# Kernel tuning notes

Hardware: AMD Instinct MI355X
Metric: run time of the kernel (lower is better)

## Reference

```python
import jax, jax.numpy as jnp
import numpy as np

D_IN, D_SAE, T, L, K = 2304, 2048, 4, 6, 128
B = 32


def setup_inputs() -> dict:
    key = jax.random.key(0)
    kx, ke, kd = jax.random.split(key, 3)
    x = jax.random.normal(kx, (B, T, L, D_IN), dtype=jnp.float32)
    W_enc = jax.random.normal(ke, (T, L, D_IN, D_SAE), dtype=jnp.float32) / np.sqrt(D_IN).astype(np.float32)
    W_dec = jax.random.normal(kd, (T, L, D_SAE, D_IN), dtype=jnp.float32) / np.sqrt(D_SAE).astype(np.float32)
    b_enc = jnp.zeros((D_SAE,), dtype=jnp.float32)
    b_dec = jnp.zeros((T, L, D_IN), dtype=jnp.float32)
    return {"x": x, "W_enc": W_enc, "W_dec": W_dec, "b_enc": b_enc, "b_dec": b_dec}


def reference(x, W_enc, W_dec, b_enc, b_dec):
    # encode: per-(t,l) matmul, pre: (B, T, L, d_sae)
    pre = jnp.einsum('btld,tlds->btls', x, W_enc) + b_enc
    Bn = pre.shape[0]
    pre_flat = pre.reshape(Bn, T * L * D_SAE)
    # global TopK over the whole (T, L, d_sae) latent grid
    v, idx = jax.lax.top_k(pre_flat, K)
    z_flat = jnp.zeros_like(pre_flat).at[jnp.arange(Bn)[:, None], idx].set(jax.nn.relu(v))
    z = z_flat.reshape(Bn, T, L, D_SAE)
    # decode: per-(t,l) matmul
    x_hat = jnp.einsum('btls,tlsd->btld', z, W_dec) + b_dec
    loss = jnp.mean(jnp.sum(jnp.square(x_hat - x), axis=-1))
    return (loss, x_hat, z)
```

## Files before the change

kernel.cpp:

```cpp
#include <hip/hip_runtime.h>

#define D_IN   2304
#define D_SAE  2048
#define TL     24
#define BATCH  32
#define K_TOP  128
#define NLAT   (TL * D_SAE)
#define NBIN   8192
#define CAP    2048
#define KSPLIT 2
#define KS     (D_IN / KSPLIT)
#define BK     32
#define NCH    (KS / BK)

typedef __attribute__((ext_vector_type(8))) short short8;
typedef __attribute__((ext_vector_type(4))) float f32x4;

__device__ __forceinline__ void async_cp16(const float* g, float* l) {
    __builtin_amdgcn_global_load_lds(
        (const __attribute__((address_space(1))) unsigned int*)g,
        (__attribute__((address_space(3))) unsigned int*)l, 16, 0, 0);
}

__device__ __forceinline__ void cvt8(const float* f, short8& hi, short8& lo) {
#pragma unroll
    for (int j = 0; j < 8; ++j) {
        unsigned u = __float_as_uint(f[j]);
        hi[j] = (short)(u >> 16);
        float l = f[j] - __uint_as_float(u & 0xFFFF0000u);
        lo[j] = (short)(__float_as_uint(l) >> 16);
    }
}

__global__ __launch_bounds__(256, 3) void enc_kernel(const float* __restrict__ x,
                                                     const float* __restrict__ W,
                                                     float* __restrict__ part) {
    __shared__ float w_s[2][BK][128];
    __shared__ float x_s[2][32][36];

    const int tid  = threadIdx.x;
    const int lane = tid & 63;
    const int wv   = tid >> 6;
    const int m0   = lane & 15;
    const int kb   = lane >> 4;
    const int tl   = blockIdx.y;
    const int ks   = blockIdx.z;
    const int n0b  = blockIdx.x * 128;
    const int kb0  = ks * KS;

    const float* Wbase = W + ((size_t)(tl * D_IN + kb0)) * D_SAE + n0b;
    const int xb = tid >> 3, xq = (tid & 7) * 4;
    const float* xsrc = x + ((size_t)(xb * TL + tl)) * D_IN + kb0 + xq;

#define STAGE_W(buf, ch)                                                        \
    do {                                                                        \
        const float* Wc = Wbase + (size_t)((ch) * BK) * D_SAE;                  \
        _Pragma("unroll")                                                       \
        for (int j = 0; j < 4; ++j) {                                           \
            int r = wv * 8 + j * 2;                                             \
            async_cp16(Wc + (size_t)(r + (lane >> 5)) * D_SAE + (lane & 31) * 4,\
                       &w_s[buf][r][0]);                                        \
        }                                                                       \
    } while (0)

    f32x4 acc[2][2];
#pragma unroll
    for (int mt = 0; mt < 2; ++mt)
#pragma unroll
        for (int nt = 0; nt < 2; ++nt) acc[mt][nt] = (f32x4)(0.f);

    {
        float4 xr = *(const float4*)xsrc;
        STAGE_W(0, 0);
        asm volatile("s_waitcnt vmcnt(0)" ::: "memory");
        *(float4*)&x_s[0][xb][xq] = xr;
        __syncthreads();
    }

    int cur = 0;
    for (int ch = 0; ch < NCH; ++ch) {
        float4 xr;
        if (ch + 1 < NCH) {
            xr = *(const float4*)(xsrc + (ch + 1) * BK);
            STAGE_W(cur ^ 1, ch + 1);
        }

        const float(*ws)[128] = w_s[cur];
        const float(*xs)[36]  = x_s[cur];
        short8 ahi[2], alo[2];
#pragma unroll
        for (int mt = 0; mt < 2; ++mt) {
            float xa[8];
            *(float4*)&xa[0] = *(const float4*)&xs[mt * 16 + m0][kb * 8];
            *(float4*)&xa[4] = *(const float4*)&xs[mt * 16 + m0][kb * 8 + 4];
            cvt8(xa, ahi[mt], alo[mt]);
        }
#pragma unroll
        for (int nt = 0; nt < 2; ++nt) {
            float wf[8];
#pragma unroll
            for (int j = 0; j < 8; ++j)
                wf[j] = ws[kb * 8 + j][wv * 32 + nt * 16 + m0];
            short8 bhi, blo;
            cvt8(wf, bhi, blo);
#pragma unroll
            for (int mt = 0; mt < 2; ++mt) {
                acc[mt][nt] = __builtin_amdgcn_mfma_f32_16x16x32_bf16(ahi[mt], bhi, acc[mt][nt], 0, 0, 0);
                acc[mt][nt] = __builtin_amdgcn_mfma_f32_16x16x32_bf16(ahi[mt], blo, acc[mt][nt], 0, 0, 0);
                acc[mt][nt] = __builtin_amdgcn_mfma_f32_16x16x32_bf16(alo[mt], bhi, acc[mt][nt], 0, 0, 0);
            }
        }

        if (ch + 1 < NCH) {
            asm volatile("s_waitcnt vmcnt(0)" ::: "memory");
            *(float4*)&x_s[cur ^ 1][xb][xq] = xr;
        }
        __syncthreads();
        cur ^= 1;
    }
#undef STAGE_W

    float* pp = part + ((size_t)ks * BATCH) * NLAT + (size_t)tl * D_SAE + n0b;
#pragma unroll
    for (int mt = 0; mt < 2; ++mt)
#pragma unroll
        for (int nt = 0; nt < 2; ++nt)
#pragma unroll
            for (int r = 0; r < 4; ++r)
                pp[(size_t)(mt * 16 + kb * 4 + r) * NLAT + wv * 32 + nt * 16 + m0] =
                    acc[mt][nt][r];
}

__global__ void reduce_kernel(const float* __restrict__ part,
                              const float* __restrict__ b_enc,
                              float* __restrict__ pre) {
    int i = (blockIdx.x * blockDim.x + threadIdx.x) * 4;
    const size_t S = (size_t)BATCH * NLAT;
    float4 v = *(const float4*)&b_enc[i & (D_SAE - 1)];
#pragma unroll
    for (int s = 0; s < KSPLIT; s++) {
        float4 p = *(const float4*)&part[i + s * S];
        v.x += p.x; v.y += p.y; v.z += p.z; v.w += p.w;
    }
    *(float4*)&pre[i] = v;
}

__global__ __launch_bounds__(256) void topk_kernel(const float* __restrict__ pre,
                                                   int* __restrict__ sel_idx,
                                                   float* __restrict__ sel_val,
                                                   float* __restrict__ z,
                                                   float* __restrict__ loss) {
    const int b   = blockIdx.x;
    const int tid = threadIdx.x;
    __shared__ unsigned hist[NBIN];
    __shared__ unsigned cand_key[CAP];
    __shared__ int      cand_idx[CAP];
    __shared__ unsigned tsum[256];
    __shared__ unsigned suf[256];
    __shared__ int s_T, s_hi, s_ccnt, s_sel;

    const float* row  = pre + (size_t)b * NLAT;
    float*       zrow = z   + (size_t)b * NLAT;
    for (int i = tid; i < NBIN; i += 256) hist[i] = 0;
    if (tid == 0) { s_ccnt = 0; s_sel = 0; if (b == 0) *loss = 0.f; }
    __syncthreads();

    for (int i = 4 * tid; i < NLAT; i += 1024) {
        float4 v = *(const float4*)&row[i];
#pragma unroll
        for (int j = 0; j < 4; j++) {
            unsigned u   = __float_as_uint(((const float*)&v)[j]);
            unsigned key = u ^ ((u >> 31) ? 0xFFFFFFFFu : 0x80000000u);
            atomicAdd(&hist[key >> 19], 1u);
        }
    }
    __syncthreads();

    unsigned local = 0;
    const int base = tid * (NBIN / 256);
    for (int j = 0; j < NBIN / 256; j++) local += hist[base + j];
    tsum[tid] = local;
    __syncthreads();
    if (tid == 0) {
        unsigned run = 0;
        for (int t = 255; t >= 0; t--) { suf[t] = run; run += tsum[t]; }
    }
    __syncthreads();
    if (suf[tid] < K_TOP && suf[tid] + tsum[tid] >= K_TOP) {
        unsigned c = suf[tid];
        for (int j = NBIN / 256 - 1; j >= 0; j--) {
            int bin = base + j;
            if (c + hist[bin] >= K_TOP) { s_T = bin; s_hi = (int)c; break; }
            c += hist[bin];
        }
    }
    __syncthreads();

    const int T = s_T;
    for (int i = 4 * tid; i < NLAT; i += 1024) {
        float4 v = *(const float4*)&row[i];
#pragma unroll
        for (int j = 0; j < 4; j++) {
            float f      = ((const float*)&v)[j];
            unsigned u   = __float_as_uint(f);
            unsigned key = u ^ ((u >> 31) ? 0xFFFFFFFFu : 0x80000000u);
            int bin      = (int)(key >> 19);
            float rl     = fmaxf(f, 0.f);
            float zval   = 0.f;
            if (bin > T) {
                int p = atomicAdd(&s_sel, 1);
                sel_idx[b * K_TOP + p] = i + j;
                sel_val[b * K_TOP + p] = rl;
                zval = rl;
            } else if (bin == T) {
                int p = atomicAdd(&s_ccnt, 1);
                if (p < CAP) { cand_key[p] = key; cand_idx[p] = i + j; }
            }
            zrow[i + j] = zval;
        }
    }
    __syncthreads();

    const int need = K_TOP - s_hi;
    const int nc   = min(s_ccnt, CAP);
    for (int c = tid; c < nc; c += 256) {
        unsigned kc = cand_key[c]; int ic = cand_idx[c];
        int rank = 0;
        for (int j = 0; j < nc; j++) {
            unsigned kj = cand_key[j]; int ij = cand_idx[j];
            rank += (kj > kc) || (kj == kc && ij < ic);
        }
        if (rank < need) {
            int p = atomicAdd(&s_sel, 1);
            float rl = fmaxf(row[ic], 0.f);
            sel_idx[b * K_TOP + p] = ic;
            sel_val[b * K_TOP + p] = rl;
            zrow[ic] = rl;
        }
    }
}

__global__ __launch_bounds__(256) void dec_kernel(const float* __restrict__ Wd,
                                                  const float* __restrict__ b_dec,
                                                  const float* __restrict__ x,
                                                  const int* __restrict__ sel_idx,
                                                  const float* __restrict__ sel_val,
                                                  float* __restrict__ xhat,
                                                  float* __restrict__ loss) {
    const int tl = blockIdx.x, b = blockIdx.y, tid = threadIdx.x;
    float acc[9];
#pragma unroll
    for (int r = 0; r < 9; r++) acc[r] = b_dec[tl * D_IN + tid + r * 256];

    __shared__ int   s_idx[K_TOP];
    __shared__ float s_val[K_TOP];
    if (tid < K_TOP) { s_idx[tid] = sel_idx[b * K_TOP + tid];
                       s_val[tid] = sel_val[b * K_TOP + tid]; }
    __syncthreads();

    for (int j = 0; j < K_TOP; j++) {
        int f = s_idx[j];
        if ((f >> 11) == tl) {
            float v = s_val[j];
            const float* wrow = Wd + (size_t)f * D_IN;
#pragma unroll
            for (int r = 0; r < 9; r++)
                acc[r] = fmaf(v, wrow[tid + r * 256], acc[r]);
        }
    }

    const float* xr = x    + ((size_t)b * TL + tl) * D_IN;
    float*       xo = xhat + ((size_t)b * TL + tl) * D_IN;
    float lsum = 0.f;
#pragma unroll
    for (int r = 0; r < 9; r++) {
        float d = acc[r] - xr[tid + r * 256];
        xo[tid + r * 256] = acc[r];
        lsum += d * d;
    }
    __shared__ float red[256];
    red[tid] = lsum; __syncthreads();
    for (int s = 128; s > 0; s >>= 1) {
        if (tid < s) red[tid] += red[tid + s];
        __syncthreads();
    }
    if (tid == 0) atomicAdd(loss, red[0] * (1.0f / (BATCH * TL)));
}

extern "C" void kernel_launch(void* const* d_in, const int* in_sizes, int n_in,
                              void* d_out, int out_size, void* d_ws, size_t ws_size,
                              hipStream_t stream) {
    const float* x     = (const float*)d_in[0];
    const float* W_enc = (const float*)d_in[1];
    const float* W_dec = (const float*)d_in[2];
    const float* b_enc = (const float*)d_in[3];
    const float* b_dec = (const float*)d_in[4];

    float* out  = (float*)d_out;
    float* loss = out;
    float* xhat = out + 1;
    float* z    = out + 1 + (size_t)BATCH * TL * D_IN;

    const size_t S = (size_t)BATCH * NLAT;
    float* part    = (float*)d_ws;
    float* pre     = part + (size_t)KSPLIT * S;
    int*   sel_idx = (int*)(pre + S);
    float* sel_val = (float*)(sel_idx + BATCH * K_TOP);

    enc_kernel<<<dim3(16, TL, KSPLIT), 256, 0, stream>>>(x, W_enc, part);
    reduce_kernel<<<(int)(S / 1024), 256, 0, stream>>>(part, b_enc, pre);
    topk_kernel<<<BATCH, 256, 0, stream>>>(pre, sel_idx, sel_val, z, loss);
    dec_kernel<<<dim3(TL, BATCH), 256, 0, stream>>>(W_dec, b_dec, x, sel_idx, sel_val,
                                                    xhat, loss);
}
```

Before: 167.2 us.

## Triple-buffer encoder W loads, read x directly to registers, widen top-k blocks

The encoder GEMM moves from double to triple buffering of W tiles in LDS, with partial vmcnt waits and a single barrier per chunk so loads stay two chunks ahead. The x operand is no longer staged through LDS; each lane loads its own fragment straight into registers. The top-k kernel goes from 256 to 512 threads per block to parallelise the histogram and scan passes over each batch row. The trade-off is more LDS and registers in the encoder, which may hurt occupancy. The loop also assumes NCH is a multiple of 3, which holds since NCH is 36.

```diff
diff --git a/kernel.cpp b/kernel.cpp
--- a/kernel.cpp
+++ b/kernel.cpp
@@ -12,6 +12,7 @@
 #define KS     (D_IN / KSPLIT)
 #define BK     32
 #define NCH    (KS / BK)
+#define TOPK_T 512
 
 typedef __attribute__((ext_vector_type(8))) short short8;
 typedef __attribute__((ext_vector_type(4))) float f32x4;
@@ -31,12 +32,16 @@
         lo[j] = (short)(__float_as_uint(l) >> 16);
     }
 }
+__device__ __forceinline__ void cvt44(float4 a, float4 b, short8& hi, short8& lo) {
+    float f[8];
+    *(float4*)&f[0] = a; *(float4*)&f[4] = b;
+    cvt8(f, hi, lo);
+}
 
 __global__ __launch_bounds__(256, 3) void enc_kernel(const float* __restrict__ x,
                                                      const float* __restrict__ W,
                                                      float* __restrict__ part) {
-    __shared__ float w_s[2][BK][128];
-    __shared__ float x_s[2][32][36];
+    __shared__ float w_s[3][BK][128];
 
     const int tid  = threadIdx.x;
     const int lane = tid & 63;
@@ -45,82 +50,78 @@
     const int kb   = lane >> 4;
     const int tl   = blockIdx.y;
     const int ks   = blockIdx.z;
-    const int n0b  = blockIdx.x * 128;
-    const int kb0  = ks * KS;
-
-    const float* Wbase = W + ((size_t)(tl * D_IN + kb0)) * D_SAE + n0b;
-    const int xb = tid >> 3, xq = (tid & 7) * 4;
-    const float* xsrc = x + ((size_t)(xb * TL + tl)) * D_IN + kb0 + xq;
-
-#define STAGE_W(buf, ch)                                                        \
+    const int col0 = blockIdx.x * 128;
+
+    const float* Wbase = W + ((size_t)(tl * D_IN + ks * KS)) * D_SAE + col0;
+    const float* xsrc0 = x + ((size_t)(m0 * TL + tl)) * D_IN + ks * KS + kb * 8;
+    const float* xsrc1 = x + ((size_t)((16 + m0) * TL + tl)) * D_IN + ks * KS + kb * 8;
+
+    float4 xr0[4], xr1[4], xr2[4];
+
+#define STAGE(BUF, CH)                                                          \
     do {                                                                        \
-        const float* Wc = Wbase + (size_t)((ch) * BK) * D_SAE;                  \
+        const float* Wc = Wbase + (size_t)(CH) * BK * D_SAE;                    \
         _Pragma("unroll")                                                       \
-        for (int j = 0; j < 4; ++j) {                                           \
-            int r = wv * 8 + j * 2;                                             \
-            async_cp16(Wc + (size_t)(r + (lane >> 5)) * D_SAE + (lane & 31) * 4,\
-                       &w_s[buf][r][0]);                                        \
+        for (int i = 0; i < 4; ++i)                                             \
+            async_cp16(Wc + (size_t)(wv * 8 + 2 * i + (lane >> 5)) * D_SAE      \
+                          + (lane & 31) * 4,                                    \
+                       &w_s[BUF][wv * 8 + 2 * i][0]);                           \
+        xr##BUF[0] = *(const float4*)(xsrc0 + (CH) * BK);                       \
+        xr##BUF[1] = *(const float4*)(xsrc0 + (CH) * BK + 4);                   \
+        xr##BUF[2] = *(const float4*)(xsrc1 + (CH) * BK);                       \
+        xr##BUF[3] = *(const float4*)(xsrc1 + (CH) * BK + 4);                   \
+    } while (0)
+
+    f32x4 acc[2][2];
+#pragma unroll
+    for (int mt = 0; mt < 2; ++mt)
+#pragma unroll
+        for (int nt = 0; nt < 2; ++nt) acc[mt][nt] = (f32x4)(0.f);
+
+#define COMPUTE(BUF)                                                            \
+    do {                                                                        \
+        const float(*ws)[128] = w_s[BUF];                                       \
+        short8 a0h, a0l, a1h, a1l;                                              \
+        cvt44(xr##BUF[0], xr##BUF[1], a0h, a0l);                                \
+        cvt44(xr##BUF[2], xr##BUF[3], a1h, a1l);                                \
+        _Pragma("unroll")                                                       \
+        for (int nt = 0; nt < 2; ++nt) {                                        \
+            float wf[8];                                                        \
+            _Pragma("unroll")                                                   \
+            for (int j = 0; j < 8; ++j)                                         \
+                wf[j] = ws[kb * 8 + j][wv * 32 + nt * 16 + m0];                 \
+            short8 bhi, blo;                                                    \
+            cvt8(wf, bhi, blo);                                                 \
+            acc[0][nt] = __builtin_amdgcn_mfma_f32_16x16x32_bf16(a0h, bhi, acc[0][nt], 0, 0, 0); \
+            acc[0][nt] = __builtin_amdgcn_mfma_f32_16x16x32_bf16(a0h, blo, acc[0][nt], 0, 0, 0); \
+            acc[0][nt] = __builtin_amdgcn_mfma_f32_16x16x32_bf16(a0l, bhi, acc[0][nt], 0, 0, 0); \
+            acc[1][nt] = __builtin_amdgcn_mfma_f32_16x16x32_bf16(a1h, bhi, acc[1][nt], 0, 0, 0); \
+            acc[1][nt] = __builtin_amdgcn_mfma_f32_16x16x32_bf16(a1h, blo, acc[1][nt], 0, 0, 0); \
+            acc[1][nt] = __builtin_amdgcn_mfma_f32_16x16x32_bf16(a1l, bhi, acc[1][nt], 0, 0, 0); \
         }                                                                       \
     } while (0)
 
-    f32x4 acc[2][2];
-#pragma unroll
-    for (int mt = 0; mt < 2; ++mt)
-#pragma unroll
-        for (int nt = 0; nt < 2; ++nt) acc[mt][nt] = (f32x4)(0.f);
-
-    {
-        float4 xr = *(const float4*)xsrc;
-        STAGE_W(0, 0);
-        asm volatile("s_waitcnt vmcnt(0)" ::: "memory");
-        *(float4*)&x_s[0][xb][xq] = xr;
-        __syncthreads();
-    }
-
-    int cur = 0;
-    for (int ch = 0; ch < NCH; ++ch) {
-        float4 xr;
-        if (ch + 1 < NCH) {
-            xr = *(const float4*)(xsrc + (ch + 1) * BK);
-            STAGE_W(cur ^ 1, ch + 1);
-        }
-
-        const float(*ws)[128] = w_s[cur];
-        const float(*xs)[36]  = x_s[cur];
-        short8 ahi[2], alo[2];
-#pragma unroll
-        for (int mt = 0; mt < 2; ++mt) {
-            float xa[8];
-            *(float4*)&xa[0] = *(const float4*)&xs[mt * 16 + m0][kb * 8];
-            *(float4*)&xa[4] = *(const float4*)&xs[mt * 16 + m0][kb * 8 + 4];
-            cvt8(xa, ahi[mt], alo[mt]);
-        }
-#pragma unroll
-        for (int nt = 0; nt < 2; ++nt) {
-            float wf[8];
-#pragma unroll
-            for (int j = 0; j < 8; ++j)
-                wf[j] = ws[kb * 8 + j][wv * 32 + nt * 16 + m0];
-            short8 bhi, blo;
-            cvt8(wf, bhi, blo);
-#pragma unroll
-            for (int mt = 0; mt < 2; ++mt) {
-                acc[mt][nt] = __builtin_amdgcn_mfma_f32_16x16x32_bf16(ahi[mt], bhi, acc[mt][nt], 0, 0, 0);
-                acc[mt][nt] = __builtin_amdgcn_mfma_f32_16x16x32_bf16(ahi[mt], blo, acc[mt][nt], 0, 0, 0);
-                acc[mt][nt] = __builtin_amdgcn_mfma_f32_16x16x32_bf16(alo[mt], bhi, acc[mt][nt], 0, 0, 0);
-            }
-        }
-
-        if (ch + 1 < NCH) {
-            asm volatile("s_waitcnt vmcnt(0)" ::: "memory");
-            *(float4*)&x_s[cur ^ 1][xb][xq] = xr;
-        }
-        __syncthreads();
-        cur ^= 1;
-    }
-#undef STAGE_W
-
-    float* pp = part + ((size_t)ks * BATCH) * NLAT + (size_t)tl * D_SAE + n0b;
+#define ITER(BUF, NXT, C)                                                       \
+    do {                                                                        \
+        if ((C) + 1 < NCH) { asm volatile("s_waitcnt vmcnt(8)" ::: "memory"); } \
+        else               { asm volatile("s_waitcnt vmcnt(0)" ::: "memory"); } \
+        __builtin_amdgcn_s_barrier();                                           \
+        if ((C) + 2 < NCH) STAGE(NXT, (C) + 2);                                 \
+        COMPUTE(BUF);                                                           \
+    } while (0)
+
+    STAGE(0, 0);
+    STAGE(1, 1);
+    for (int c3 = 0; c3 < NCH; c3 += 3) {
+        ITER(0, 2, c3);
+        ITER(1, 0, c3 + 1);
+        ITER(2, 1, c3 + 2);
+    }
+#undef ITER
+#undef COMPUTE
+#undef STAGE
+
+    float* pp = part + ((size_t)ks * BATCH) * NLAT + (size_t)tl * D_SAE + col0;
 #pragma unroll
     for (int mt = 0; mt < 2; ++mt)
 #pragma unroll
@@ -145,27 +146,27 @@
     *(float4*)&pre[i] = v;
 }
 
-__global__ __launch_bounds__(256) void topk_kernel(const float* __restrict__ pre,
-                                                   int* __restrict__ sel_idx,
-                                                   float* __restrict__ sel_val,
-                                                   float* __restrict__ z,
-                                                   float* __restrict__ loss) {
+__global__ __launch_bounds__(TOPK_T) void topk_kernel(const float* __restrict__ pre,
+                                                      int* __restrict__ sel_idx,
+                                                      float* __restrict__ sel_val,
+                                                      float* __restrict__ z,
+                                                      float* __restrict__ loss) {
     const int b   = blockIdx.x;
     const int tid = threadIdx.x;
     __shared__ unsigned hist[NBIN];
     __shared__ unsigned cand_key[CAP];
     __shared__ int      cand_idx[CAP];
-    __shared__ unsigned tsum[256];
-    __shared__ unsigned suf[256];
+    __shared__ unsigned tsum[TOPK_T];
+    __shared__ unsigned suf[TOPK_T];
     __shared__ int s_T, s_hi, s_ccnt, s_sel;
 
     const float* row  = pre + (size_t)b * NLAT;
     float*       zrow = z   + (size_t)b * NLAT;
-    for (int i = tid; i < NBIN; i += 256) hist[i] = 0;
+    for (int i = tid; i < NBIN; i += TOPK_T) hist[i] = 0;
     if (tid == 0) { s_ccnt = 0; s_sel = 0; if (b == 0) *loss = 0.f; }
     __syncthreads();
 
-    for (int i = 4 * tid; i < NLAT; i += 1024) {
+    for (int i = 4 * tid; i < NLAT; i += 4 * TOPK_T) {
         float4 v = *(const float4*)&row[i];
 #pragma unroll
         for (int j = 0; j < 4; j++) {
@@ -177,18 +178,18 @@
     __syncthreads();
 
     unsigned local = 0;
-    const int base = tid * (NBIN / 256);
-    for (int j = 0; j < NBIN / 256; j++) local += hist[base + j];
+    const int base = tid * (NBIN / TOPK_T);
+    for (int j = 0; j < NBIN / TOPK_T; j++) local += hist[base + j];
     tsum[tid] = local;
     __syncthreads();
     if (tid == 0) {
         unsigned run = 0;
-        for (int t = 255; t >= 0; t--) { suf[t] = run; run += tsum[t]; }
+        for (int t = TOPK_T - 1; t >= 0; t--) { suf[t] = run; run += tsum[t]; }
     }
     __syncthreads();
     if (suf[tid] < K_TOP && suf[tid] + tsum[tid] >= K_TOP) {
         unsigned c = suf[tid];
-        for (int j = NBIN / 256 - 1; j >= 0; j--) {
+        for (int j = NBIN / TOPK_T - 1; j >= 0; j--) {
             int bin = base + j;
             if (c + hist[bin] >= K_TOP) { s_T = bin; s_hi = (int)c; break; }
             c += hist[bin];
@@ -197,7 +198,7 @@
     __syncthreads();
 
     const int T = s_T;
-    for (int i = 4 * tid; i < NLAT; i += 1024) {
+    for (int i = 4 * tid; i < NLAT; i += 4 * TOPK_T) {
         float4 v = *(const float4*)&row[i];
 #pragma unroll
         for (int j = 0; j < 4; j++) {
@@ -223,7 +224,7 @@
 
     const int need = K_TOP - s_hi;
     const int nc   = min(s_ccnt, CAP);
-    for (int c = tid; c < nc; c += 256) {
+    for (int c = tid; c < nc; c += TOPK_T) {
         unsigned kc = cand_key[c]; int ic = cand_idx[c];
         int rank = 0;
         for (int j = 0; j < nc; j++) {
@@ -309,7 +310,7 @@
 
     enc_kernel<<<dim3(16, TL, KSPLIT), 256, 0, stream>>>(x, W_enc, part);
     reduce_kernel<<<(int)(S / 1024), 256, 0, stream>>>(part, b_enc, pre);
-    topk_kernel<<<BATCH, 256, 0, stream>>>(pre, sel_idx, sel_val, z, loss);
+    topk_kernel<<<BATCH, TOPK_T, 0, stream>>>(pre, sel_idx, sel_val, z, loss);
     dec_kernel<<<dim3(TL, BATCH), 256, 0, stream>>>(W_dec, b_dec, x, sel_idx, sel_val,
                                                     xhat, loss);
 }
```

New measurement: 165.0 us. Within noise of the previous version (-1.3%).
